# Performance work log

Hardware: AMD Instinct MI355X
Metric: run time of the kernel (lower is better)

## Reference

```python
import jax, jax.numpy as jnp
import numpy as np

N_POINTS = 1048576
FEATURES = 64
RES = 256


def setup_inputs() -> dict:
    key = jax.random.key(0)
    k1, k2, k3, k4 = jax.random.split(key, 4)
    x = jax.random.uniform(k1, (N_POINTS, 3), jnp.float32, -1.0, 1.0)
    plane_xy = jax.random.normal(k2, (1, FEATURES, RES, RES), jnp.float32)
    plane_xz = jax.random.normal(k3, (1, FEATURES, RES, RES), jnp.float32)
    plane_yz = jax.random.normal(k4, (1, FEATURES, RES, RES), jnp.float32)
    pose = jnp.zeros((1,), jnp.float32)
    person_id = 0
    return {"x": x, "plane_xy": plane_xy, "plane_xz": plane_xz,
            "plane_yz": plane_yz, "pose": pose, "person_id": person_id}


def _grid_sample_points(plane, uv):
    """Bilinear sample. plane: [1,C,IH,IW], uv: [N,2] in [-1,1]. Returns [N,C].
    Matches the hand-rolled torch grid_sample (align_corners=True semantics,
    corner indices clamped, weights computed from unclamped floor coords)."""
    C, IH, IW = plane.shape[1], plane.shape[2], plane.shape[3]
    ix = (uv[:, 0] + 1.0) * 0.5 * (IW - 1)
    iy = (uv[:, 1] + 1.0) * 0.5 * (IH - 1)
    fx0 = jnp.floor(ix)
    fy0 = jnp.floor(iy)
    # bilinear weights (differentiable w.r.t. ix, iy)
    w_nw = (fx0 + 1.0 - ix) * (fy0 + 1.0 - iy)
    w_ne = (ix - fx0) * (fy0 + 1.0 - iy)
    w_sw = (fx0 + 1.0 - ix) * (iy - fy0)
    w_se = (ix - fx0) * (iy - fy0)
    # clamped integer corner indices (non-differentiable, as in torch no_grad)
    x0 = jnp.clip(fx0, 0, IW - 1).astype(jnp.int32)
    x1 = jnp.clip(fx0 + 1.0, 0, IW - 1).astype(jnp.int32)
    y0 = jnp.clip(fy0, 0, IH - 1).astype(jnp.int32)
    y1 = jnp.clip(fy0 + 1.0, 0, IH - 1).astype(jnp.int32)
    pf = plane.reshape(C, IH * IW)  # [C, IH*IW]
    v_nw = pf[:, y0 * IW + x0]  # [C, N]
    v_ne = pf[:, y0 * IW + x1]
    v_sw = pf[:, y1 * IW + x0]
    v_se = pf[:, y1 * IW + x1]
    out = v_nw * w_nw + v_ne * w_ne + v_sw * w_sw + v_se * w_se  # [C, N]
    return out.T  # [N, C]


def reference(x, plane_xy, plane_xz, plane_yz, pose, person_id):
    # person_id selects the (single) person's planes; pose is unused upstream.
    feat_xy = _grid_sample_points(plane_xy, x[:, [0, 1]])
    feat_xz = _grid_sample_points(plane_xz, x[:, [0, 2]])
    feat_yz = _grid_sample_points(plane_yz, x[:, [1, 2]])
    feat = (feat_xy + feat_xz + feat_yz) / 3.0  # [N, FEATURES]
    return feat
```

## Files before the change

kernel.cpp:

```cpp
#include <hip/hip_runtime.h>

#define N_POINTS 1048576
#define FEAT 64
#define RES 256
#define PLANE_ELEMS (FEAT * RES * RES)

#define BUCKET_G 32
#define NBUCKET (BUCKET_G * BUCKET_G * BUCKET_G)

#define SAMPLE_BLOCKS (N_POINTS / 32)
#define SAMPLE_CPX (SAMPLE_BLOCKS / 8)

#define TRANSPOSE_BLOCKS (3 * (RES * RES / 64))
#define COUNT_BLOCKS (N_POINTS / 256)
#define PREP_BLOCKS (TRANSPOSE_BLOCKS + COUNT_BLOCKS)

typedef unsigned short ushort_t;
typedef float v4f __attribute__((ext_vector_type(4)));
typedef _Float16 half8 __attribute__((ext_vector_type(8)));

__device__ __forceinline__ ushort_t f2h(float f) {
  _Float16 h = (_Float16)f;
  return __builtin_bit_cast(unsigned short, h);
}

__device__ __forceinline__ unsigned part1by2(unsigned v) {
  v &= 0x3FFu;
  v = (v | (v << 16)) & 0x030000FFu;
  v = (v | (v << 8)) & 0x0300F00Fu;
  v = (v | (v << 4)) & 0x030C30C3u;
  v = (v | (v << 2)) & 0x09249249u;
  return v;
}

__device__ __forceinline__ unsigned morton_bucket(float px, float py, float pz) {
  int bx = (int)((px + 1.0f) * (0.5f * BUCKET_G));
  int by = (int)((py + 1.0f) * (0.5f * BUCKET_G));
  int bz = (int)((pz + 1.0f) * (0.5f * BUCKET_G));
  bx = min(max(bx, 0), BUCKET_G - 1);
  by = min(max(by, 0), BUCKET_G - 1);
  bz = min(max(bz, 0), BUCKET_G - 1);
  return part1by2((unsigned)bx) | (part1by2((unsigned)by) << 1) |
         (part1by2((unsigned)bz) << 2);
}

__global__ __launch_bounds__(256) void prep_transpose_count(
    const float* __restrict__ pxy, const float* __restrict__ pxz,
    const float* __restrict__ pyz, ushort_t* __restrict__ dst,
    const float* __restrict__ x, unsigned* __restrict__ hist) {
  const int b = blockIdx.x;
  const int tid = threadIdx.x;
  if (b >= TRANSPOSE_BLOCKS) {
    int n = (b - TRANSPOSE_BLOCKS) * 256 + tid;
    float px = x[n * 3 + 0];
    float py = x[n * 3 + 1];
    float pz = x[n * 3 + 2];
    atomicAdd(&hist[morton_bucket(px, py, pz)], 1u);
    return;
  }
  __shared__ ushort_t tile[64][72];
  const int plane = b >> 10;
  const int p0 = (b & 1023) * 64;
  const float* src = (plane == 0) ? pxy : ((plane == 1) ? pxz : pyz);
  ushort_t* out = dst + (size_t)plane * PLANE_ELEMS;
#pragma unroll
  for (int k = 0; k < 4; ++k) {
    int c = (tid >> 4) + k * 16;
    int pp = (tid & 15) * 4;
    v4f v = __builtin_nontemporal_load(
        (const v4f*)(src + (size_t)c * (RES * RES) + p0 + pp));
    tile[pp + 0][c] = f2h(v.x);
    tile[pp + 1][c] = f2h(v.y);
    tile[pp + 2][c] = f2h(v.z);
    tile[pp + 3][c] = f2h(v.w);
  }
  __syncthreads();
#pragma unroll
  for (int k = 0; k < 2; ++k) {
    int idx = k * 256 + tid;
    int pp = idx >> 3;
    int c8 = (idx & 7) * 8;
    uint4 v = *(const uint4*)&tile[pp][c8];
    *(uint4*)(out + (size_t)(p0 + pp) * FEAT + c8) = v;
  }
}

__global__ __launch_bounds__(1024) void scan_hist(
    const unsigned* __restrict__ hist, unsigned* __restrict__ cursor) {
  __shared__ unsigned part[1024];
  const int tid = threadIdx.x;
  unsigned local[32];
  unsigned s = 0;
#pragma unroll
  for (int i = 0; i < 32; ++i) {
    local[i] = s;
    s += hist[tid * 32 + i];
  }
  part[tid] = s;
  __syncthreads();
  for (int off = 1; off < 1024; off <<= 1) {
    unsigned add = (tid >= off) ? part[tid - off] : 0u;
    __syncthreads();
    part[tid] += add;
    __syncthreads();
  }
  unsigned base = (tid == 0) ? 0u : part[tid - 1];
#pragma unroll
  for (int i = 0; i < 32; ++i) cursor[tid * 32 + i] = base + local[i];
}

__global__ __launch_bounds__(256) void bucket_scatter(
    const float* __restrict__ x, unsigned* __restrict__ cursor,
    float4* __restrict__ xs) {
  int n = blockIdx.x * 256 + threadIdx.x;
  float px = x[n * 3 + 0];
  float py = x[n * 3 + 1];
  float pz = x[n * 3 + 2];
  unsigned b = morton_bucket(px, py, pz);
  unsigned pos = atomicAdd(&cursor[b], 1u);
  xs[pos] = make_float4(px, py, pz, __uint_as_float((unsigned)n));
}

__device__ __forceinline__ void fma_mix8(half8 v, float w, float* acc) {
#pragma unroll
  for (int j = 0; j < 8; ++j) acc[j] = fmaf((float)v[j], w, acc[j]);
}

__device__ __forceinline__ void sample_plane(const ushort_t* __restrict__ tp,
                                             float u, float v, int c8,
                                             float* acc) {
  float ix = fmaf(u, 0.5f * (float)(RES - 1), 0.5f * (float)(RES - 1));
  float iy = fmaf(v, 0.5f * (float)(RES - 1), 0.5f * (float)(RES - 1));
  float fx0 = floorf(ix), fy0 = floorf(iy);
  float wx1 = ix - fx0, wy1 = iy - fy0;
  float wx0 = fx0 + 1.0f - ix, wy0 = fy0 + 1.0f - iy;
  int x0 = min(max((int)fx0, 0), RES - 1);
  int y0 = min(max((int)fy0, 0), RES - 1);
  int x1 = min(max((int)fx0 + 1, 0), RES - 1);
  int y1 = min(max((int)fy0 + 1, 0), RES - 1);

  const half8 v00 = *(const half8*)(tp + (size_t)(y0 * RES + x0) * FEAT + c8);
  const half8 v01 = *(const half8*)(tp + (size_t)(y0 * RES + x1) * FEAT + c8);
  const half8 v10 = *(const half8*)(tp + (size_t)(y1 * RES + x0) * FEAT + c8);
  const half8 v11 = *(const half8*)(tp + (size_t)(y1 * RES + x1) * FEAT + c8);

  fma_mix8(v00, wx0 * wy0, acc);
  fma_mix8(v01, wx1 * wy0, acc);
  fma_mix8(v10, wx0 * wy1, acc);
  fma_mix8(v11, wx1 * wy1, acc);
}

__global__ __launch_bounds__(256) void triplane_sample_sorted(
    const float4* __restrict__ xs, const ushort_t* __restrict__ tps,
    float* __restrict__ out) {
  int bid = blockIdx.x;
  int swz = (bid & 7) * SAMPLE_CPX + (bid >> 3);
  int p = swz * 32 + (threadIdx.x >> 3);
  int c8 = (threadIdx.x & 7) << 3;

  v4f pt = __builtin_nontemporal_load((const v4f*)xs + p);
  unsigned n = __float_as_uint(pt.w);

  float acc[8] = {0.f, 0.f, 0.f, 0.f, 0.f, 0.f, 0.f, 0.f};
  sample_plane(tps, pt.x, pt.y, c8, acc);
  sample_plane(tps + PLANE_ELEMS, pt.x, pt.z, c8, acc);
  sample_plane(tps + 2 * PLANE_ELEMS, pt.y, pt.z, c8, acc);

  const float s = 1.0f / 3.0f;
  v4f lo = {acc[0] * s, acc[1] * s, acc[2] * s, acc[3] * s};
  v4f hi = {acc[4] * s, acc[5] * s, acc[6] * s, acc[7] * s};
  float* o = out + (size_t)n * FEAT + c8;
  __builtin_nontemporal_store(lo, (v4f*)o);
  __builtin_nontemporal_store(hi, (v4f*)(o + 4));
}

__global__ __launch_bounds__(256) void transpose_only(
    const float* __restrict__ pxy, const float* __restrict__ pxz,
    const float* __restrict__ pyz, ushort_t* __restrict__ dst) {
  __shared__ ushort_t tile[64][72];
  const int plane = blockIdx.y;
  const float* src = (plane == 0) ? pxy : ((plane == 1) ? pxz : pyz);
  ushort_t* out = dst + (size_t)plane * PLANE_ELEMS;
  const int p0 = blockIdx.x * 64;
  const int tid = threadIdx.x;
#pragma unroll
  for (int k = 0; k < 4; ++k) {
    int c = (tid >> 4) + k * 16;
    int pp = (tid & 15) * 4;
    v4f v = *(const v4f*)(src + (size_t)c * (RES * RES) + p0 + pp);
    tile[pp + 0][c] = f2h(v.x);
    tile[pp + 1][c] = f2h(v.y);
    tile[pp + 2][c] = f2h(v.z);
    tile[pp + 3][c] = f2h(v.w);
  }
  __syncthreads();
#pragma unroll
  for (int k = 0; k < 2; ++k) {
    int idx = k * 256 + tid;
    int pp = idx >> 3;
    int c8 = (idx & 7) * 8;
    uint4 v = *(const uint4*)&tile[pp][c8];
    *(uint4*)(out + (size_t)(p0 + pp) * FEAT + c8) = v;
  }
}

__global__ __launch_bounds__(256) void triplane_sample_f16(
    const float* __restrict__ x, const ushort_t* __restrict__ tps,
    float* __restrict__ out) {
  int t = blockIdx.x * 256 + threadIdx.x;
  int n = t >> 3;
  int c8 = (t & 7) << 3;
  float px = __builtin_nontemporal_load(x + n * 3 + 0);
  float py = __builtin_nontemporal_load(x + n * 3 + 1);
  float pz = __builtin_nontemporal_load(x + n * 3 + 2);
  float acc[8] = {0.f, 0.f, 0.f, 0.f, 0.f, 0.f, 0.f, 0.f};
  sample_plane(tps, px, py, c8, acc);
  sample_plane(tps + PLANE_ELEMS, px, pz, c8, acc);
  sample_plane(tps + 2 * PLANE_ELEMS, py, pz, c8, acc);
  const float s = 1.0f / 3.0f;
  v4f lo = {acc[0] * s, acc[1] * s, acc[2] * s, acc[3] * s};
  v4f hi = {acc[4] * s, acc[5] * s, acc[6] * s, acc[7] * s};
  float* o = out + (size_t)n * FEAT + c8;
  __builtin_nontemporal_store(lo, (v4f*)o);
  __builtin_nontemporal_store(hi, (v4f*)(o + 4));
}

__device__ __forceinline__ float sample_one(const float* __restrict__ pc,
                                            float u, float v) {
  float ix = (u + 1.0f) * 0.5f * (float)(RES - 1);
  float iy = (v + 1.0f) * 0.5f * (float)(RES - 1);
  float fx0 = floorf(ix), fy0 = floorf(iy);
  float wx1 = ix - fx0, wy1 = iy - fy0;
  float wx0 = fx0 + 1.0f - ix, wy0 = fy0 + 1.0f - iy;
  int x0 = min(max((int)fx0, 0), RES - 1);
  int y0 = min(max((int)fy0, 0), RES - 1);
  int x1 = min(max((int)fx0 + 1, 0), RES - 1);
  int y1 = min(max((int)fy0 + 1, 0), RES - 1);
  return pc[y0 * RES + x0] * (wx0 * wy0) + pc[y0 * RES + x1] * (wx1 * wy0) +
         pc[y1 * RES + x0] * (wx0 * wy1) + pc[y1 * RES + x1] * (wx1 * wy1);
}

__global__ __launch_bounds__(256) void triplane_direct(
    const float* __restrict__ x, const float* __restrict__ pxy,
    const float* __restrict__ pxz, const float* __restrict__ pyz,
    float* __restrict__ out) {
  int t = blockIdx.x * 256 + threadIdx.x;
  int n = t >> 6;
  int c = t & 63;
  float px = x[n * 3 + 0];
  float py = x[n * 3 + 1];
  float pz = x[n * 3 + 2];
  const size_t cs = (size_t)c * (RES * RES);
  float acc = sample_one(pxy + cs, px, py) + sample_one(pxz + cs, px, pz) +
              sample_one(pyz + cs, py, pz);
  out[(size_t)n * FEAT + c] = acc * (1.0f / 3.0f);
}

extern "C" void kernel_launch(void* const* d_in, const int* in_sizes, int n_in,
                              void* d_out, int out_size, void* d_ws,
                              size_t ws_size, hipStream_t stream) {
  const float* x   = (const float*)d_in[0];
  const float* pxy = (const float*)d_in[1];
  const float* pxz = (const float*)d_in[2];
  const float* pyz = (const float*)d_in[3];
  float* out = (float*)d_out;

  const size_t tps_bytes = (size_t)3 * PLANE_ELEMS * sizeof(ushort_t);
  const size_t xs_bytes  = (size_t)N_POINTS * sizeof(float4);
  const size_t cnt_bytes = (size_t)NBUCKET * sizeof(unsigned);
  const size_t need_sorted = tps_bytes + xs_bytes + 2 * cnt_bytes;

  if (ws_size >= need_sorted) {
    ushort_t* tps    = (ushort_t*)d_ws;
    float4* xs       = (float4*)((char*)d_ws + tps_bytes);
    unsigned* cursor = (unsigned*)((char*)d_ws + tps_bytes + xs_bytes);
    unsigned* hist   = cursor + NBUCKET;

    (void)hipMemsetAsync(hist, 0, cnt_bytes, stream);
    prep_transpose_count<<<PREP_BLOCKS, 256, 0, stream>>>(pxy, pxz, pyz, tps,
                                                          x, hist);
    scan_hist<<<1, 1024, 0, stream>>>(hist, cursor);
    bucket_scatter<<<N_POINTS / 256, 256, 0, stream>>>(x, cursor, xs);
    triplane_sample_sorted<<<SAMPLE_BLOCKS, 256, 0, stream>>>(xs, tps, out);
  } else if (ws_size >= tps_bytes) {
    ushort_t* tps = (ushort_t*)d_ws;
    dim3 tgrid(RES * RES / 64, 3);
    transpose_only<<<tgrid, 256, 0, stream>>>(pxy, pxz, pyz, tps);
    triplane_sample_f16<<<(N_POINTS * 8) / 256, 256, 0, stream>>>(x, tps, out);
  } else {
    triplane_direct<<<(N_POINTS * 64) / 256, 256, 0, stream>>>(x, pxy, pxz,
                                                               pyz, out);
  }
}
```

Before: 472.5 us.

## Stage per-bucket plane footprints in LDS and sample sorted points from shared memory

Coarsens the spatial buckets to 16^3 and launches one 512-thread block per bucket. Each block first copies the 18x18 texel footprint of all three fp16 planes into LDS, then bilinearly samples every point in its bucket from LDS instead of issuing scattered global gathers. The scan now also writes bucket start offsets, and the post-scatter cursor serves as the end offsets. The cost is about 124 KB of LDS per block, which limits occupancy, plus uneven work across blocks because bucket sizes vary.

```diff
diff --git a/kernel.cpp b/kernel.cpp
--- a/kernel.cpp
+++ b/kernel.cpp
@@ -5,11 +5,13 @@
 #define RES 256
 #define PLANE_ELEMS (FEAT * RES * RES)
 
-#define BUCKET_G 32
+#define BUCKET_G 16
 #define NBUCKET (BUCKET_G * BUCKET_G * BUCKET_G)
 
-#define SAMPLE_BLOCKS (N_POINTS / 32)
-#define SAMPLE_CPX (SAMPLE_BLOCKS / 8)
+#define FOOT 18
+#define FOOT2 (FOOT * FOOT)
+#define LDS_PLANE (FOOT2 * FEAT)
+#define STAGE_U4 (3 * FOOT2 * FEAT / 8)
 
 #define TRANSPOSE_BLOCKS (3 * (RES * RES / 64))
 #define COUNT_BLOCKS (N_POINTS / 256)
@@ -30,6 +32,15 @@
   v = (v | (v << 8)) & 0x0300F00Fu;
   v = (v | (v << 4)) & 0x030C30C3u;
   v = (v | (v << 2)) & 0x09249249u;
+  return v;
+}
+
+__device__ __forceinline__ unsigned compact1by2(unsigned v) {
+  v &= 0x09249249u;
+  v = (v | (v >> 2)) & 0x030C30C3u;
+  v = (v | (v >> 4)) & 0x0300F00Fu;
+  v = (v | (v >> 8)) & 0x030000FFu;
+  v = (v | (v >> 16)) & 0x3FFu;
   return v;
 }
 
@@ -86,16 +97,13 @@
 }
 
 __global__ __launch_bounds__(1024) void scan_hist(
-    const unsigned* __restrict__ hist, unsigned* __restrict__ cursor) {
+    const uint4* __restrict__ hist4, unsigned* __restrict__ starts,
+    unsigned* __restrict__ cursor) {
   __shared__ unsigned part[1024];
   const int tid = threadIdx.x;
-  unsigned local[32];
-  unsigned s = 0;
-#pragma unroll
-  for (int i = 0; i < 32; ++i) {
-    local[i] = s;
-    s += hist[tid * 32 + i];
-  }
+  uint4 h = hist4[tid];
+  unsigned l0 = 0, l1 = h.x, l2 = h.x + h.y, l3 = h.x + h.y + h.z;
+  unsigned s = l3 + h.w;
   part[tid] = s;
   __syncthreads();
   for (int off = 1; off < 1024; off <<= 1) {
@@ -105,8 +113,13 @@
     __syncthreads();
   }
   unsigned base = (tid == 0) ? 0u : part[tid - 1];
-#pragma unroll
-  for (int i = 0; i < 32; ++i) cursor[tid * 32 + i] = base + local[i];
+  uint4 o;
+  o.x = base + l0;
+  o.y = base + l1;
+  o.z = base + l2;
+  o.w = base + l3;
+  ((uint4*)starts)[tid] = o;
+  ((uint4*)cursor)[tid] = o;
 }
 
 __global__ __launch_bounds__(256) void bucket_scatter(
@@ -121,14 +134,149 @@
   xs[pos] = make_float4(px, py, pz, __uint_as_float((unsigned)n));
 }
 
+__device__ __forceinline__ void plane_lds_ref(float u, float v, int rb, int cb,
+                                              int c8, int* off, float* w) {
+  float ix = fmaf(u, 0.5f * (float)(RES - 1), 0.5f * (float)(RES - 1));
+  float iy = fmaf(v, 0.5f * (float)(RES - 1), 0.5f * (float)(RES - 1));
+  float fx0 = floorf(ix), fy0 = floorf(iy);
+  float wx1 = ix - fx0, wy1 = iy - fy0;
+  float wx0 = fx0 + 1.0f - ix, wy0 = fy0 + 1.0f - iy;
+  int x0 = min(max((int)fx0, 0), RES - 1) - cb;
+  int y0 = min(max((int)fy0, 0), RES - 1) - rb;
+  int x1 = min(max((int)fx0 + 1, 0), RES - 1) - cb;
+  int y1 = min(max((int)fy0 + 1, 0), RES - 1) - rb;
+  off[0] = (y0 * FOOT + x0) * FEAT + c8;
+  off[1] = (y0 * FOOT + x1) * FEAT + c8;
+  off[2] = (y1 * FOOT + x0) * FEAT + c8;
+  off[3] = (y1 * FOOT + x1) * FEAT + c8;
+  w[0] = wx0 * wy0;
+  w[1] = wx1 * wy0;
+  w[2] = wx0 * wy1;
+  w[3] = wx1 * wy1;
+}
+
 __device__ __forceinline__ void fma_mix8(half8 v, float w, float* acc) {
 #pragma unroll
   for (int j = 0; j < 8; ++j) acc[j] = fmaf((float)v[j], w, acc[j]);
 }
 
-__device__ __forceinline__ void sample_plane(const ushort_t* __restrict__ tp,
-                                             float u, float v, int c8,
-                                             float* acc) {
+__global__ __launch_bounds__(512) void triplane_sample_lds(
+    const float4* __restrict__ xs, const ushort_t* __restrict__ tps,
+    const unsigned* __restrict__ starts, const unsigned* __restrict__ ends,
+    float* __restrict__ out) {
+  __shared__ __align__(16) ushort_t lds[3 * LDS_PLANE];
+  const int tid = threadIdx.x;
+  const int bid = blockIdx.x;
+  const int b = (bid & 7) * (NBUCKET / 8) + (bid >> 3);
+  const int bx = (int)compact1by2((unsigned)b);
+  const int by = (int)compact1by2((unsigned)b >> 1);
+  const int bz = (int)compact1by2((unsigned)b >> 2);
+  const int xb = (255 * bx) >> 4;
+  const int yb = (255 * by) >> 4;
+  const int zb = (255 * bz) >> 4;
+
+  uint4* l4 = (uint4*)lds;
+  for (int f = tid; f < STAGE_U4; f += 512) {
+    int p = f / (FOOT2 * 8);
+    int rem = f - p * (FOOT2 * 8);
+    int t = rem >> 3;
+    int sub = rem & 7;
+    int row = t / FOOT;
+    int col = t - row * FOOT;
+    int rb = (p == 0) ? yb : zb;
+    int cb = (p == 2) ? yb : xb;
+    int gr = min(rb + row, RES - 1);
+    int gc = min(cb + col, RES - 1);
+    l4[f] = *(const uint4*)(tps + (size_t)p * PLANE_ELEMS +
+                            ((gr << 8) + gc) * FEAT + sub * 8);
+  }
+  __syncthreads();
+
+  const unsigned s0 = starts[b], e0 = ends[b];
+  const int c8 = (tid & 7) << 3;
+  const ushort_t* l0 = lds;
+  const ushort_t* l1 = lds + LDS_PLANE;
+  const ushort_t* l2 = lds + 2 * LDS_PLANE;
+
+  for (unsigned pid = s0 + (tid >> 3); pid < e0; pid += 64) {
+    v4f pt = __builtin_nontemporal_load((const v4f*)xs + pid);
+    unsigned n = __float_as_uint(pt.w);
+
+    int oa[4], ob[4], oc[4];
+    float wa[4], wb[4], wc[4];
+    plane_lds_ref(pt.x, pt.y, yb, xb, c8, oa, wa);
+    plane_lds_ref(pt.x, pt.z, zb, xb, c8, ob, wb);
+    plane_lds_ref(pt.y, pt.z, zb, yb, c8, oc, wc);
+
+    const half8 a00 = *(const half8*)(l0 + oa[0]);
+    const half8 a01 = *(const half8*)(l0 + oa[1]);
+    const half8 a10 = *(const half8*)(l0 + oa[2]);
+    const half8 a11 = *(const half8*)(l0 + oa[3]);
+    const half8 b00 = *(const half8*)(l1 + ob[0]);
+    const half8 b01 = *(const half8*)(l1 + ob[1]);
+    const half8 b10 = *(const half8*)(l1 + ob[2]);
+    const half8 b11 = *(const half8*)(l1 + ob[3]);
+    const half8 c00 = *(const half8*)(l2 + oc[0]);
+    const half8 c01 = *(const half8*)(l2 + oc[1]);
+    const half8 c10 = *(const half8*)(l2 + oc[2]);
+    const half8 c11 = *(const half8*)(l2 + oc[3]);
+
+    float acc[8] = {0.f, 0.f, 0.f, 0.f, 0.f, 0.f, 0.f, 0.f};
+    fma_mix8(a00, wa[0], acc);
+    fma_mix8(a01, wa[1], acc);
+    fma_mix8(a10, wa[2], acc);
+    fma_mix8(a11, wa[3], acc);
+    fma_mix8(b00, wb[0], acc);
+    fma_mix8(b01, wb[1], acc);
+    fma_mix8(b10, wb[2], acc);
+    fma_mix8(b11, wb[3], acc);
+    fma_mix8(c00, wc[0], acc);
+    fma_mix8(c01, wc[1], acc);
+    fma_mix8(c10, wc[2], acc);
+    fma_mix8(c11, wc[3], acc);
+
+    const float s = 1.0f / 3.0f;
+    v4f lo = {acc[0] * s, acc[1] * s, acc[2] * s, acc[3] * s};
+    v4f hi = {acc[4] * s, acc[5] * s, acc[6] * s, acc[7] * s};
+    float* o = out + (size_t)n * FEAT + c8;
+    __builtin_nontemporal_store(lo, (v4f*)o);
+    __builtin_nontemporal_store(hi, (v4f*)(o + 4));
+  }
+}
+
+__global__ __launch_bounds__(256) void transpose_only(
+    const float* __restrict__ pxy, const float* __restrict__ pxz,
+    const float* __restrict__ pyz, ushort_t* __restrict__ dst) {
+  __shared__ ushort_t tile[64][72];
+  const int plane = blockIdx.y;
+  const float* src = (plane == 0) ? pxy : ((plane == 1) ? pxz : pyz);
+  ushort_t* out = dst + (size_t)plane * PLANE_ELEMS;
+  const int p0 = blockIdx.x * 64;
+  const int tid = threadIdx.x;
+#pragma unroll
+  for (int k = 0; k < 4; ++k) {
+    int c = (tid >> 4) + k * 16;
+    int pp = (tid & 15) * 4;
+    v4f v = *(const v4f*)(src + (size_t)c * (RES * RES) + p0 + pp);
+    tile[pp + 0][c] = f2h(v.x);
+    tile[pp + 1][c] = f2h(v.y);
+    tile[pp + 2][c] = f2h(v.z);
+    tile[pp + 3][c] = f2h(v.w);
+  }
+  __syncthreads();
+#pragma unroll
+  for (int k = 0; k < 2; ++k) {
+    int idx = k * 256 + tid;
+    int pp = idx >> 3;
+    int c8 = (idx & 7) * 8;
+    uint4 v = *(const uint4*)&tile[pp][c8];
+    *(uint4*)(out + (size_t)(p0 + pp) * FEAT + c8) = v;
+  }
+}
+
+__device__ __forceinline__ void sample_plane_g(const ushort_t* __restrict__ tp,
+                                               float u, float v, int c8,
+                                               float* acc) {
   float ix = fmaf(u, 0.5f * (float)(RES - 1), 0.5f * (float)(RES - 1));
   float iy = fmaf(v, 0.5f * (float)(RES - 1), 0.5f * (float)(RES - 1));
   float fx0 = floorf(ix), fy0 = floorf(iy);
@@ -138,70 +286,14 @@
   int y0 = min(max((int)fy0, 0), RES - 1);
   int x1 = min(max((int)fx0 + 1, 0), RES - 1);
   int y1 = min(max((int)fy0 + 1, 0), RES - 1);
-
   const half8 v00 = *(const half8*)(tp + (size_t)(y0 * RES + x0) * FEAT + c8);
   const half8 v01 = *(const half8*)(tp + (size_t)(y0 * RES + x1) * FEAT + c8);
   const half8 v10 = *(const half8*)(tp + (size_t)(y1 * RES + x0) * FEAT + c8);
   const half8 v11 = *(const half8*)(tp + (size_t)(y1 * RES + x1) * FEAT + c8);
-
   fma_mix8(v00, wx0 * wy0, acc);
   fma_mix8(v01, wx1 * wy0, acc);
   fma_mix8(v10, wx0 * wy1, acc);
   fma_mix8(v11, wx1 * wy1, acc);
-}
-
-__global__ __launch_bounds__(256) void triplane_sample_sorted(
-    const float4* __restrict__ xs, const ushort_t* __restrict__ tps,
-    float* __restrict__ out) {
-  int bid = blockIdx.x;
-  int swz = (bid & 7) * SAMPLE_CPX + (bid >> 3);
-  int p = swz * 32 + (threadIdx.x >> 3);
-  int c8 = (threadIdx.x & 7) << 3;
-
-  v4f pt = __builtin_nontemporal_load((const v4f*)xs + p);
-  unsigned n = __float_as_uint(pt.w);
-
-  float acc[8] = {0.f, 0.f, 0.f, 0.f, 0.f, 0.f, 0.f, 0.f};
-  sample_plane(tps, pt.x, pt.y, c8, acc);
-  sample_plane(tps + PLANE_ELEMS, pt.x, pt.z, c8, acc);
-  sample_plane(tps + 2 * PLANE_ELEMS, pt.y, pt.z, c8, acc);
-
-  const float s = 1.0f / 3.0f;
-  v4f lo = {acc[0] * s, acc[1] * s, acc[2] * s, acc[3] * s};
-  v4f hi = {acc[4] * s, acc[5] * s, acc[6] * s, acc[7] * s};
-  float* o = out + (size_t)n * FEAT + c8;
-  __builtin_nontemporal_store(lo, (v4f*)o);
-  __builtin_nontemporal_store(hi, (v4f*)(o + 4));
-}
-
-__global__ __launch_bounds__(256) void transpose_only(
-    const float* __restrict__ pxy, const float* __restrict__ pxz,
-    const float* __restrict__ pyz, ushort_t* __restrict__ dst) {
-  __shared__ ushort_t tile[64][72];
-  const int plane = blockIdx.y;
-  const float* src = (plane == 0) ? pxy : ((plane == 1) ? pxz : pyz);
-  ushort_t* out = dst + (size_t)plane * PLANE_ELEMS;
-  const int p0 = blockIdx.x * 64;
-  const int tid = threadIdx.x;
-#pragma unroll
-  for (int k = 0; k < 4; ++k) {
-    int c = (tid >> 4) + k * 16;
-    int pp = (tid & 15) * 4;
-    v4f v = *(const v4f*)(src + (size_t)c * (RES * RES) + p0 + pp);
-    tile[pp + 0][c] = f2h(v.x);
-    tile[pp + 1][c] = f2h(v.y);
-    tile[pp + 2][c] = f2h(v.z);
-    tile[pp + 3][c] = f2h(v.w);
-  }
-  __syncthreads();
-#pragma unroll
-  for (int k = 0; k < 2; ++k) {
-    int idx = k * 256 + tid;
-    int pp = idx >> 3;
-    int c8 = (idx & 7) * 8;
-    uint4 v = *(const uint4*)&tile[pp][c8];
-    *(uint4*)(out + (size_t)(p0 + pp) * FEAT + c8) = v;
-  }
 }
 
 __global__ __launch_bounds__(256) void triplane_sample_f16(
@@ -214,9 +306,9 @@
   float py = __builtin_nontemporal_load(x + n * 3 + 1);
   float pz = __builtin_nontemporal_load(x + n * 3 + 2);
   float acc[8] = {0.f, 0.f, 0.f, 0.f, 0.f, 0.f, 0.f, 0.f};
-  sample_plane(tps, px, py, c8, acc);
-  sample_plane(tps + PLANE_ELEMS, px, pz, c8, acc);
-  sample_plane(tps + 2 * PLANE_ELEMS, py, pz, c8, acc);
+  sample_plane_g(tps, px, py, c8, acc);
+  sample_plane_g(tps + PLANE_ELEMS, px, pz, c8, acc);
+  sample_plane_g(tps + 2 * PLANE_ELEMS, py, pz, c8, acc);
   const float s = 1.0f / 3.0f;
   v4f lo = {acc[0] * s, acc[1] * s, acc[2] * s, acc[3] * s};
   v4f hi = {acc[4] * s, acc[5] * s, acc[6] * s, acc[7] * s};
@@ -268,20 +360,22 @@
   const size_t tps_bytes = (size_t)3 * PLANE_ELEMS * sizeof(ushort_t);
   const size_t xs_bytes  = (size_t)N_POINTS * sizeof(float4);
   const size_t cnt_bytes = (size_t)NBUCKET * sizeof(unsigned);
-  const size_t need_sorted = tps_bytes + xs_bytes + 2 * cnt_bytes;
+  const size_t need_sorted = tps_bytes + xs_bytes + 3 * cnt_bytes;
 
   if (ws_size >= need_sorted) {
     ushort_t* tps    = (ushort_t*)d_ws;
     float4* xs       = (float4*)((char*)d_ws + tps_bytes);
     unsigned* cursor = (unsigned*)((char*)d_ws + tps_bytes + xs_bytes);
     unsigned* hist   = cursor + NBUCKET;
+    unsigned* starts = hist + NBUCKET;
 
     (void)hipMemsetAsync(hist, 0, cnt_bytes, stream);
     prep_transpose_count<<<PREP_BLOCKS, 256, 0, stream>>>(pxy, pxz, pyz, tps,
                                                           x, hist);
-    scan_hist<<<1, 1024, 0, stream>>>(hist, cursor);
+    scan_hist<<<1, 1024, 0, stream>>>((const uint4*)hist, starts, cursor);
     bucket_scatter<<<N_POINTS / 256, 256, 0, stream>>>(x, cursor, xs);
-    triplane_sample_sorted<<<SAMPLE_BLOCKS, 256, 0, stream>>>(xs, tps, out);
+    triplane_sample_lds<<<NBUCKET, 512, 0, stream>>>(xs, tps, starts, cursor,
+                                                     out);
   } else if (ws_size >= tps_bytes) {
     ushort_t* tps = (ushort_t*)d_ws;
     dim3 tgrid(RES * RES / 64, 3);
```

Result: slower. 570.6 us (+20.8%).
